# Performance work log

Measured on AMD Instinct MI355X. Metric: run time of the kernel, lower is better.

Reference implementation:

```python
import jax, jax.numpy as jnp
import numpy as np

N = 100000      # nodes
NNZ = 1600000   # edges (avg degree 16)
F_IN = 128
F_OUT = 128


def setup_inputs() -> dict:
    key = jax.random.key(0)
    ks = jax.random.split(key, 8)
    return {
        "features": jax.random.normal(ks[0], (N, F_IN), dtype=jnp.float32),
        "edge_val": jax.random.uniform(ks[1], (NNZ,), dtype=jnp.float32),
        "W1": jax.random.normal(ks[2], (F_IN, F_OUT), dtype=jnp.float32) * 0.05,
        "b1": jax.random.normal(ks[3], (F_OUT,), dtype=jnp.float32) * 0.05,
        "W2": jax.random.normal(ks[4], (F_IN, F_OUT), dtype=jnp.float32) * 0.05,
        "b2": jax.random.normal(ks[5], (F_OUT,), dtype=jnp.float32) * 0.05,
        "edge_row": jax.random.randint(ks[6], (NNZ,), 0, N, dtype=jnp.int32),
        "edge_col": jax.random.randint(ks[7], (NNZ,), 0, N, dtype=jnp.int32),
    }


def _spmm(edge_val, edge_row, edge_col, x, n):
    # sparse (n,n) COO matrix @ dense (n,f): gather cols, scale, scatter-add rows
    gathered = edge_val[:, None] * x[edge_col]          # (nnz, f)
    return jax.ops.segment_sum(gathered, edge_row, num_segments=n)


def reference(features, edge_val, W1, b1, W2, b2, edge_row, edge_col):
    n = features.shape[0]
    Lf = _spmm(edge_val, edge_row, edge_col, features, n)   # L2 @ features
    inter_feature = Lf * features                            # elementwise mul
    # L1 = L + I, so L1 @ features == Lf + features (selfLoop is identity)
    inter_part1 = (Lf + features) @ W1 + b1                  # self.linear
    Li = _spmm(edge_val, edge_row, edge_col, inter_feature, n)
    inter_part2 = Li @ W2 + b2                               # interActTransform
    return inter_part1 + inter_part2
```

## Files before the change

kernel.cpp:

```cpp
#include <hip/hip_runtime.h>

#define F 128
#define NBSHIFT 7
#define CAPB 3072
#define CHUNK 8192

typedef __attribute__((ext_vector_type(8))) short bf16x8;
typedef __attribute__((ext_vector_type(4))) float f32x4;

__device__ inline float bf2f(unsigned short u) {
    union { unsigned int i; float f; } x;
    x.i = ((unsigned int)u) << 16;
    return x.f;
}
__device__ inline unsigned short f2bf(float f) {
    union { float f; unsigned int i; } x;
    x.f = f;
    unsigned int lsb = (x.i >> 16) & 1;
    x.i += 0x7FFFu + lsb;
    return (unsigned short)(x.i >> 16);
}

__global__ __launch_bounds__(256) void convert_feat(
    const float* __restrict__ feat, unsigned short* __restrict__ feat_h, int total4)
{
    int i = blockIdx.x * 256 + threadIdx.x;
    if (i >= total4) return;
    float4 v = *(const float4*)(feat + (size_t)i * 4);
    ushort4 o;
    o.x = f2bf(v.x); o.y = f2bf(v.y); o.z = f2bf(v.z); o.w = f2bf(v.w);
    *(ushort4*)(feat_h + (size_t)i * 4) = o;
}

__global__ __launch_bounds__(256) void pack_W(
    const float* __restrict__ W1, const float* __restrict__ W2,
    unsigned short* __restrict__ Wp)
{
    int idx = blockIdx.x * 256 + threadIdx.x;
    if (idx >= 8 * 8 * 64) return;
    int lane = idx & 63;
    int ks   = (idx >> 6) & 7;
    int nt   = idx >> 9;
    int col  = nt * 16 + (lane & 15);
    int krow = ks * 32 + (lane >> 4) * 8;
    const float* W = (krow < 128) ? (W1 + (size_t)krow * F)
                                  : (W2 + (size_t)(krow - 128) * F);
    unsigned short o[8];
#pragma unroll
    for (int j = 0; j < 8; ++j) o[j] = f2bf(W[(size_t)j * F + col]);
    unsigned short* dst = Wp + (size_t)idx * 8;
    *(ushort4*)(dst)     = make_ushort4(o[0], o[1], o[2], o[3]);
    *(ushort4*)(dst + 4) = make_ushort4(o[4], o[5], o[6], o[7]);
}

__global__ __launch_bounds__(256) void bin_edges(
    const int* __restrict__ er, const int* __restrict__ ec,
    const float* __restrict__ ev,
    int* __restrict__ gcnt, uint2* __restrict__ gbuf, int nnz, int nb)
{
    __shared__ int hist[1024];
    __shared__ int base[1024];
    const int tid  = threadIdx.x;
    const int e0   = blockIdx.x * CHUNK;
    const int eend = min(e0 + CHUNK, nnz);

    for (int b = tid; b < nb; b += 256) hist[b] = 0;
    __syncthreads();

    for (int e = e0 + tid; e < eend; e += 256) {
        int b = er[e] >> NBSHIFT;
        atomicAdd(&hist[b], 1);
    }
    __syncthreads();

    for (int b = tid; b < nb; b += 256) {
        int h = hist[b];
        base[b] = h ? atomicAdd(&gcnt[b], h) : 0;
        hist[b] = 0;
    }
    __syncthreads();

    for (int e = e0 + tid; e < eend; e += 256) {
        int r = er[e];
        int b = r >> NBSHIFT;
        int rank = atomicAdd(&hist[b], 1);
        int idx  = base[b] + rank;
        if (idx >= CAPB) idx = CAPB - 1;
        unsigned int q = (unsigned int)__float2int_rn(ev[e] * 32767.f);
        gbuf[(size_t)b * CAPB + idx] =
            make_uint2((q << 17) | (unsigned int)ec[e], (unsigned int)r);
    }
}

__global__ __launch_bounds__(256) void bucket_to_rows(
    const int* __restrict__ gcnt, const uint2* __restrict__ gbuf,
    int* __restrict__ cnt, unsigned int* __restrict__ recs, int n, int cap)
{
    __shared__ unsigned int slots[128][64];
    __shared__ int lcnt[128];
    const int b = blockIdx.x;
    const int tid = threadIdx.x;
    const int base_row = b << NBSHIFT;

    for (int r = tid; r < 128; r += 256) lcnt[r] = 0;
    __syncthreads();

    int nrec = gcnt[b];
    if (nrec > CAPB) nrec = CAPB;
    const uint2* gb = gbuf + (size_t)b * CAPB;
    for (int i = tid; i < nrec; i += 256) {
        uint2 rec = gb[i];
        int r = (int)rec.y - base_row;
        int pos = atomicAdd(&lcnt[r], 1);
        if (pos < cap) slots[r][pos] = rec.x;
    }
    __syncthreads();

    int r = tid >> 1;
    int row = base_row + r;
    if (row < n) {
        int c = lcnt[r];
        if (c > cap) c = cap;
        if ((tid & 1) == 0) cnt[row] = c;
        unsigned int* dst = recs + (size_t)row * cap;
        for (int i = tid & 1; i < c; i += 2) dst[i] = slots[r][i];
    }
}

__global__ __launch_bounds__(256) void spmm_feat(
    const unsigned short* __restrict__ feat_h, const float* __restrict__ feat,
    const int* __restrict__ cnt, const unsigned int* __restrict__ recs,
    unsigned short* __restrict__ A1_h, unsigned short* __restrict__ P_h,
    int n, int cap)
{
    int gid = blockIdx.x * 256 + threadIdx.x;
    int row = gid >> 5;
    if (row >= n) return;
    int f = (gid & 31) << 2;
    const unsigned int* rp = recs + (size_t)row * cap;
    int e = cnt[row];
    if (e > cap) e = cap;

    float4 acc0 = {0.f, 0.f, 0.f, 0.f};
    float4 acc1 = {0.f, 0.f, 0.f, 0.f};
    int i = 0;
    for (; i + 1 < e; i += 2) {
        unsigned int u0 = rp[i];
        unsigned int u1 = rp[i + 1];
        float v0 = (float)(u0 >> 17) * (1.f / 32767.f);
        float v1 = (float)(u1 >> 17) * (1.f / 32767.f);
        ushort4 x0 = *(const ushort4*)(feat_h + (size_t)(u0 & 0x1FFFF) * F + f);
        ushort4 x1 = *(const ushort4*)(feat_h + (size_t)(u1 & 0x1FFFF) * F + f);
        acc0.x += v0 * bf2f(x0.x);
        acc0.y += v0 * bf2f(x0.y);
        acc0.z += v0 * bf2f(x0.z);
        acc0.w += v0 * bf2f(x0.w);
        acc1.x += v1 * bf2f(x1.x);
        acc1.y += v1 * bf2f(x1.y);
        acc1.z += v1 * bf2f(x1.z);
        acc1.w += v1 * bf2f(x1.w);
    }
    if (i < e) {
        unsigned int u0 = rp[i];
        float v0 = (float)(u0 >> 17) * (1.f / 32767.f);
        ushort4 x0 = *(const ushort4*)(feat_h + (size_t)(u0 & 0x1FFFF) * F + f);
        acc0.x += v0 * bf2f(x0.x);
        acc0.y += v0 * bf2f(x0.y);
        acc0.z += v0 * bf2f(x0.z);
        acc0.w += v0 * bf2f(x0.w);
    }
    float4 acc;
    acc.x = acc0.x + acc1.x;
    acc.y = acc0.y + acc1.y;
    acc.z = acc0.z + acc1.z;
    acc.w = acc0.w + acc1.w;

    size_t o = (size_t)row * F + f;
    float4 ft = *(const float4*)(feat + o);

    ushort4 a1;
    a1.x = f2bf(acc.x + ft.x);
    a1.y = f2bf(acc.y + ft.y);
    a1.z = f2bf(acc.z + ft.z);
    a1.w = f2bf(acc.w + ft.w);
    *(ushort4*)(A1_h + o) = a1;

    ushort4 ph;
    ph.x = f2bf(acc.x * ft.x);
    ph.y = f2bf(acc.y * ft.y);
    ph.z = f2bf(acc.z * ft.z);
    ph.w = f2bf(acc.w * ft.w);
    *(ushort4*)(P_h + o) = ph;
}

__global__ __launch_bounds__(256) void spmm_inter(
    const unsigned short* __restrict__ P_h,
    const int* __restrict__ cnt, const unsigned int* __restrict__ recs,
    unsigned short* __restrict__ Li_h, int n, int cap)
{
    int gid = blockIdx.x * 256 + threadIdx.x;
    int row = gid >> 5;
    if (row >= n) return;
    int f = (gid & 31) << 2;
    const unsigned int* rp = recs + (size_t)row * cap;
    int e = cnt[row];
    if (e > cap) e = cap;

    float4 acc0 = {0.f, 0.f, 0.f, 0.f};
    float4 acc1 = {0.f, 0.f, 0.f, 0.f};
    int i = 0;
    for (; i + 1 < e; i += 2) {
        unsigned int u0 = rp[i];
        unsigned int u1 = rp[i + 1];
        float v0 = (float)(u0 >> 17) * (1.f / 32767.f);
        float v1 = (float)(u1 >> 17) * (1.f / 32767.f);
        ushort4 x0 = *(const ushort4*)(P_h + (size_t)(u0 & 0x1FFFF) * F + f);
        ushort4 x1 = *(const ushort4*)(P_h + (size_t)(u1 & 0x1FFFF) * F + f);
        acc0.x += v0 * bf2f(x0.x);
        acc0.y += v0 * bf2f(x0.y);
        acc0.z += v0 * bf2f(x0.z);
        acc0.w += v0 * bf2f(x0.w);
        acc1.x += v1 * bf2f(x1.x);
        acc1.y += v1 * bf2f(x1.y);
        acc1.z += v1 * bf2f(x1.z);
        acc1.w += v1 * bf2f(x1.w);
    }
    if (i < e) {
        unsigned int u0 = rp[i];
        float v0 = (float)(u0 >> 17) * (1.f / 32767.f);
        ushort4 x0 = *(const ushort4*)(P_h + (size_t)(u0 & 0x1FFFF) * F + f);
        acc0.x += v0 * bf2f(x0.x);
        acc0.y += v0 * bf2f(x0.y);
        acc0.z += v0 * bf2f(x0.z);
        acc0.w += v0 * bf2f(x0.w);
    }
    ushort4 lh;
    lh.x = f2bf(acc0.x + acc1.x);
    lh.y = f2bf(acc0.y + acc1.y);
    lh.z = f2bf(acc0.z + acc1.z);
    lh.w = f2bf(acc0.w + acc1.w);
    *(ushort4*)(Li_h + (size_t)row * F + f) = lh;
}

__global__ __launch_bounds__(256) void gemm_mfma(
    const unsigned short* __restrict__ A1_h,
    const unsigned short* __restrict__ Li_h,
    const unsigned short* __restrict__ Wp,
    const float* __restrict__ b1, const float* __restrict__ b2,
    float* __restrict__ out, int n)
{
    const int wave = threadIdx.x >> 6;
    const int lane = threadIdx.x & 63;
    const int quad = lane >> 4;
    const int l16  = lane & 15;
    const int row0 = blockIdx.x * 64 + wave * 16;

    int arow = row0 + l16;
    if (arow >= n) arow = n - 1;

    f32x4 acc[8];
#pragma unroll
    for (int t = 0; t < 8; ++t) acc[t] = (f32x4){0.f, 0.f, 0.f, 0.f};

    const unsigned short* A1p = A1_h + (size_t)arow * F + quad * 8;
    const unsigned short* A2p = Li_h + (size_t)arow * F + quad * 8;

#pragma unroll
    for (int ks = 0; ks < 8; ++ks) {
        const unsigned short* ap = (ks < 4) ? (A1p + ks * 32) : (A2p + (ks - 4) * 32);
        bf16x8 a = *(const bf16x8*)ap;
#pragma unroll
        for (int t = 0; t < 8; ++t) {
            bf16x8 b = *(const bf16x8*)(Wp + ((size_t)(t * 8 + ks) * 64 + lane) * 8);
            acc[t] = __builtin_amdgcn_mfma_f32_16x16x32_bf16(a, b, acc[t], 0, 0, 0);
        }
    }

    const int orow0 = row0 + quad * 4;
#pragma unroll
    for (int t = 0; t < 8; ++t) {
        int col = t * 16 + l16;
        float bias = b1[col] + b2[col];
#pragma unroll
        for (int r = 0; r < 4; ++r) {
            int gr = orow0 + r;
            if (gr < n) out[(size_t)gr * F + col] = acc[t][r] + bias;
        }
    }
}

extern "C" void kernel_launch(void* const* d_in, const int* in_sizes, int n_in,
                              void* d_out, int out_size, void* d_ws, size_t ws_size,
                              hipStream_t stream)
{
    const float* feat = (const float*)d_in[0];
    const float* ev   = (const float*)d_in[1];
    const float* W1   = (const float*)d_in[2];
    const float* b1   = (const float*)d_in[3];
    const float* W2   = (const float*)d_in[4];
    const float* b2   = (const float*)d_in[5];
    const int*   er   = (const int*)d_in[6];
    const int*   ec   = (const int*)d_in[7];

    const int n   = in_sizes[0] / F;
    const int nnz = in_sizes[1];
    int nb = (n + 127) >> NBSHIFT;
    if (nb > 1024) nb = 1024;

    char* ws = (char*)d_ws;
    unsigned short* feat_h = (unsigned short*)ws;  ws += (size_t)n * F * sizeof(short);
    unsigned short* A1_h   = (unsigned short*)ws;  ws += (size_t)n * F * sizeof(short);
    unsigned short* P_h    = (unsigned short*)ws;  ws += (size_t)n * F * sizeof(short);
    unsigned short* Li_h   = (unsigned short*)ws;  ws += (size_t)n * F * sizeof(short);
    unsigned short* Wp     = (unsigned short*)ws;  ws += (size_t)8 * 8 * 64 * 8 * sizeof(short);
    int* cnt               = (int*)ws;             ws += (size_t)n * sizeof(int);
    int* gcnt              = (int*)ws;             ws += (size_t)nb * sizeof(int);
    unsigned int* recs     = (unsigned int*)ws;

    uint2* gbuf = (uint2*)Li_h;

    size_t used  = (size_t)(ws - (char*)d_ws);
    size_t avail = (ws_size > used) ? (ws_size - used) : 0;
    int cap = (int)(avail / ((size_t)n * sizeof(unsigned int)));
    if (cap > 64) cap = 64;

    hipMemsetAsync(gcnt, 0, (size_t)nb * sizeof(int), stream);

    const int total4 = n * F / 4;

    convert_feat<<<(total4 + 255) / 256, 256, 0, stream>>>(feat, feat_h, total4);
    pack_W<<<16, 256, 0, stream>>>(W1, W2, Wp);

    bin_edges<<<(nnz + CHUNK - 1) / CHUNK, 256, 0, stream>>>(er, ec, ev, gcnt,
                                                             gbuf, nnz, nb);
    bucket_to_rows<<<nb, 256, 0, stream>>>(gcnt, gbuf, cnt, recs, n, cap);

    int spmm_blocks = (n * 32 + 255) / 256;
    spmm_feat<<<spmm_blocks, 256, 0, stream>>>(feat_h, feat, cnt, recs,
                                               A1_h, P_h, n, cap);
    spmm_inter<<<spmm_blocks, 256, 0, stream>>>(P_h, cnt, recs, Li_h, n, cap);

    gemm_mfma<<<(n + 63) / 64, 256, 0, stream>>>(A1_h, Li_h, Wp, b1, b2,
                                                 (float*)d_out, n);
}
```

Baseline: 388.3 us.

## Fuse prep kernels, vectorize row record stores, and unroll SpMM gathers by eight

Feature conversion, weight packing and edge binning now run as one launch, with block index ranges choosing the job. Binning keeps row ids in registers instead of reading them twice. Row records are written with 128-bit stores from a padded shared tile, with cap rounded down to a multiple of four. The SpMM gather loop loads records as uint4 and issues eight independent feature gathers into four accumulators, to get more memory requests in flight. The costs are more register pressure and a less balanced fused launch.

```diff
diff --git a/kernel.cpp b/kernel.cpp
--- a/kernel.cpp
+++ b/kernel.cpp
@@ -4,6 +4,7 @@
 #define NBSHIFT 7
 #define CAPB 3072
 #define CHUNK 8192
+#define NBMAX 1024
 
 typedef __attribute__((ext_vector_type(8))) short bf16x8;
 typedef __attribute__((ext_vector_type(4))) float f32x4;
@@ -21,74 +22,81 @@
     return (unsigned short)(x.i >> 16);
 }
 
-__global__ __launch_bounds__(256) void convert_feat(
-    const float* __restrict__ feat, unsigned short* __restrict__ feat_h, int total4)
-{
-    int i = blockIdx.x * 256 + threadIdx.x;
-    if (i >= total4) return;
-    float4 v = *(const float4*)(feat + (size_t)i * 4);
-    ushort4 o;
-    o.x = f2bf(v.x); o.y = f2bf(v.y); o.z = f2bf(v.z); o.w = f2bf(v.w);
-    *(ushort4*)(feat_h + (size_t)i * 4) = o;
-}
-
-__global__ __launch_bounds__(256) void pack_W(
+__global__ __launch_bounds__(256) void prep(
+    const float* __restrict__ feat, unsigned short* __restrict__ feat_h, int total4,
     const float* __restrict__ W1, const float* __restrict__ W2,
-    unsigned short* __restrict__ Wp)
-{
-    int idx = blockIdx.x * 256 + threadIdx.x;
-    if (idx >= 8 * 8 * 64) return;
-    int lane = idx & 63;
-    int ks   = (idx >> 6) & 7;
-    int nt   = idx >> 9;
-    int col  = nt * 16 + (lane & 15);
-    int krow = ks * 32 + (lane >> 4) * 8;
-    const float* W = (krow < 128) ? (W1 + (size_t)krow * F)
-                                  : (W2 + (size_t)(krow - 128) * F);
-    unsigned short o[8];
-#pragma unroll
-    for (int j = 0; j < 8; ++j) o[j] = f2bf(W[(size_t)j * F + col]);
-    unsigned short* dst = Wp + (size_t)idx * 8;
-    *(ushort4*)(dst)     = make_ushort4(o[0], o[1], o[2], o[3]);
-    *(ushort4*)(dst + 4) = make_ushort4(o[4], o[5], o[6], o[7]);
-}
-
-__global__ __launch_bounds__(256) void bin_edges(
+    unsigned short* __restrict__ Wp,
     const int* __restrict__ er, const int* __restrict__ ec,
     const float* __restrict__ ev,
-    int* __restrict__ gcnt, uint2* __restrict__ gbuf, int nnz, int nb)
-{
-    __shared__ int hist[1024];
-    __shared__ int base[1024];
-    const int tid  = threadIdx.x;
-    const int e0   = blockIdx.x * CHUNK;
-    const int eend = min(e0 + CHUNK, nnz);
-
-    for (int b = tid; b < nb; b += 256) hist[b] = 0;
-    __syncthreads();
-
-    for (int e = e0 + tid; e < eend; e += 256) {
-        int b = er[e] >> NBSHIFT;
-        atomicAdd(&hist[b], 1);
-    }
-    __syncthreads();
-
-    for (int b = tid; b < nb; b += 256) {
-        int h = hist[b];
-        base[b] = h ? atomicAdd(&gcnt[b], h) : 0;
-        hist[b] = 0;
-    }
-    __syncthreads();
-
-    for (int e = e0 + tid; e < eend; e += 256) {
-        int r = er[e];
-        int b = r >> NBSHIFT;
-        int rank = atomicAdd(&hist[b], 1);
-        int idx  = base[b] + rank;
-        if (idx >= CAPB) idx = CAPB - 1;
-        unsigned int q = (unsigned int)__float2int_rn(ev[e] * 32767.f);
-        gbuf[(size_t)b * CAPB + idx] =
-            make_uint2((q << 17) | (unsigned int)ec[e], (unsigned int)r);
+    int* __restrict__ gcnt, uint2* __restrict__ gbuf, int nnz, int nb, int nbin)
+{
+    __shared__ int hist[NBMAX];
+    __shared__ int base[NBMAX];
+    const int bid = blockIdx.x;
+    const int tid = threadIdx.x;
+
+    if (bid < nbin) {
+        const int e0 = bid * CHUNK;
+        int rreg[32];
+
+        for (int b = tid; b < nb; b += 256) hist[b] = 0;
+        __syncthreads();
+
+#pragma unroll
+        for (int k = 0; k < 32; ++k) {
+            int e = e0 + k * 256 + tid;
+            int r = (e < nnz) ? er[e] : -1;
+            rreg[k] = r;
+            if (r >= 0) atomicAdd(&hist[r >> NBSHIFT], 1);
+        }
+        __syncthreads();
+
+        for (int b = tid; b < nb; b += 256) {
+            int h = hist[b];
+            base[b] = h ? atomicAdd(&gcnt[b], h) : 0;
+            hist[b] = 0;
+        }
+        __syncthreads();
+
+#pragma unroll
+        for (int k = 0; k < 32; ++k) {
+            int r = rreg[k];
+            if (r >= 0) {
+                int e = e0 + k * 256 + tid;
+                int b = r >> NBSHIFT;
+                int rank = atomicAdd(&hist[b], 1);
+                int idx  = base[b] + rank;
+                if (idx >= CAPB) idx = CAPB - 1;
+                unsigned int q = (unsigned int)__float2int_rn(ev[e] * 32767.f);
+                gbuf[(size_t)b * CAPB + idx] =
+                    make_uint2((q << 17) | (unsigned int)ec[e], (unsigned int)r);
+            }
+        }
+    } else if (bid < nbin + 16) {
+        int idx = (bid - nbin) * 256 + tid;
+        if (idx < 8 * 8 * 64) {
+            int lane = idx & 63;
+            int ks   = (idx >> 6) & 7;
+            int nt   = idx >> 9;
+            int col  = nt * 16 + (lane & 15);
+            int krow = ks * 32 + (lane >> 4) * 8;
+            const float* W = (krow < 128) ? (W1 + (size_t)krow * F)
+                                          : (W2 + (size_t)(krow - 128) * F);
+            unsigned short o[8];
+#pragma unroll
+            for (int j = 0; j < 8; ++j) o[j] = f2bf(W[(size_t)j * F + col]);
+            unsigned short* dst = Wp + (size_t)idx * 8;
+            *(ushort4*)(dst)     = make_ushort4(o[0], o[1], o[2], o[3]);
+            *(ushort4*)(dst + 4) = make_ushort4(o[4], o[5], o[6], o[7]);
+        }
+    } else {
+        int i = (bid - nbin - 16) * 256 + tid;
+        if (i < total4) {
+            float4 v = *(const float4*)(feat + (size_t)i * 4);
+            ushort4 o;
+            o.x = f2bf(v.x); o.y = f2bf(v.y); o.z = f2bf(v.z); o.w = f2bf(v.w);
+            *(ushort4*)(feat_h + (size_t)i * 4) = o;
+        }
     }
 }
 
@@ -96,7 +104,7 @@
     const int* __restrict__ gcnt, const uint2* __restrict__ gbuf,
     int* __restrict__ cnt, unsigned int* __restrict__ recs, int n, int cap)
 {
-    __shared__ unsigned int slots[128][64];
+    __shared__ unsigned int slots[128][68];
     __shared__ int lcnt[128];
     const int b = blockIdx.x;
     const int tid = threadIdx.x;
@@ -116,15 +124,94 @@
     }
     __syncthreads();
 
-    int r = tid >> 1;
-    int row = base_row + r;
-    if (row < n) {
-        int c = lcnt[r];
+    const int sub = tid & 3;
+    for (int rr = tid >> 2; rr < 128; rr += 64) {
+        int row = base_row + rr;
+        if (row >= n) continue;
+        int c = lcnt[rr];
         if (c > cap) c = cap;
-        if ((tid & 1) == 0) cnt[row] = c;
-        unsigned int* dst = recs + (size_t)row * cap;
-        for (int i = tid & 1; i < c; i += 2) dst[i] = slots[r][i];
-    }
+        if (sub == 0) cnt[row] = c;
+        uint4* dst = (uint4*)(recs + (size_t)row * cap);
+        for (int q = sub; q * 4 < c; q += 4)
+            dst[q] = *(const uint4*)&slots[rr][q * 4];
+    }
+}
+
+__device__ inline float4 row_gather(
+    const unsigned short* __restrict__ src,
+    const unsigned int* __restrict__ rp, int e, int f)
+{
+    float4 A0 = {0.f,0.f,0.f,0.f}, A1 = {0.f,0.f,0.f,0.f};
+    float4 A2 = {0.f,0.f,0.f,0.f}, A3 = {0.f,0.f,0.f,0.f};
+    int i = 0;
+    for (; i + 7 < e; i += 8) {
+        uint4 ua = *(const uint4*)(rp + i);
+        uint4 ub = *(const uint4*)(rp + i + 4);
+        ushort4 x0 = *(const ushort4*)(src + (size_t)(ua.x & 0x1FFFF) * F + f);
+        ushort4 x1 = *(const ushort4*)(src + (size_t)(ua.y & 0x1FFFF) * F + f);
+        ushort4 x2 = *(const ushort4*)(src + (size_t)(ua.z & 0x1FFFF) * F + f);
+        ushort4 x3 = *(const ushort4*)(src + (size_t)(ua.w & 0x1FFFF) * F + f);
+        ushort4 x4 = *(const ushort4*)(src + (size_t)(ub.x & 0x1FFFF) * F + f);
+        ushort4 x5 = *(const ushort4*)(src + (size_t)(ub.y & 0x1FFFF) * F + f);
+        ushort4 x6 = *(const ushort4*)(src + (size_t)(ub.z & 0x1FFFF) * F + f);
+        ushort4 x7 = *(const ushort4*)(src + (size_t)(ub.w & 0x1FFFF) * F + f);
+        float v0 = (float)(ua.x >> 17) * (1.f / 32767.f);
+        float v1 = (float)(ua.y >> 17) * (1.f / 32767.f);
+        float v2 = (float)(ua.z >> 17) * (1.f / 32767.f);
+        float v3 = (float)(ua.w >> 17) * (1.f / 32767.f);
+        float v4 = (float)(ub.x >> 17) * (1.f / 32767.f);
+        float v5 = (float)(ub.y >> 17) * (1.f / 32767.f);
+        float v6 = (float)(ub.z >> 17) * (1.f / 32767.f);
+        float v7 = (float)(ub.w >> 17) * (1.f / 32767.f);
+        A0.x += v0 * bf2f(x0.x); A0.y += v0 * bf2f(x0.y);
+        A0.z += v0 * bf2f(x0.z); A0.w += v0 * bf2f(x0.w);
+        A1.x += v1 * bf2f(x1.x); A1.y += v1 * bf2f(x1.y);
+        A1.z += v1 * bf2f(x1.z); A1.w += v1 * bf2f(x1.w);
+        A2.x += v2 * bf2f(x2.x); A2.y += v2 * bf2f(x2.y);
+        A2.z += v2 * bf2f(x2.z); A2.w += v2 * bf2f(x2.w);
+        A3.x += v3 * bf2f(x3.x); A3.y += v3 * bf2f(x3.y);
+        A3.z += v3 * bf2f(x3.z); A3.w += v3 * bf2f(x3.w);
+        A0.x += v4 * bf2f(x4.x); A0.y += v4 * bf2f(x4.y);
+        A0.z += v4 * bf2f(x4.z); A0.w += v4 * bf2f(x4.w);
+        A1.x += v5 * bf2f(x5.x); A1.y += v5 * bf2f(x5.y);
+        A1.z += v5 * bf2f(x5.z); A1.w += v5 * bf2f(x5.w);
+        A2.x += v6 * bf2f(x6.x); A2.y += v6 * bf2f(x6.y);
+        A2.z += v6 * bf2f(x6.z); A2.w += v6 * bf2f(x6.w);
+        A3.x += v7 * bf2f(x7.x); A3.y += v7 * bf2f(x7.y);
+        A3.z += v7 * bf2f(x7.z); A3.w += v7 * bf2f(x7.w);
+    }
+    for (; i + 3 < e; i += 4) {
+        uint4 ua = *(const uint4*)(rp + i);
+        ushort4 x0 = *(const ushort4*)(src + (size_t)(ua.x & 0x1FFFF) * F + f);
+        ushort4 x1 = *(const ushort4*)(src + (size_t)(ua.y & 0x1FFFF) * F + f);
+        ushort4 x2 = *(const ushort4*)(src + (size_t)(ua.z & 0x1FFFF) * F + f);
+        ushort4 x3 = *(const ushort4*)(src + (size_t)(ua.w & 0x1FFFF) * F + f);
+        float v0 = (float)(ua.x >> 17) * (1.f / 32767.f);
+        float v1 = (float)(ua.y >> 17) * (1.f / 32767.f);
+        float v2 = (float)(ua.z >> 17) * (1.f / 32767.f);
+        float v3 = (float)(ua.w >> 17) * (1.f / 32767.f);
+        A0.x += v0 * bf2f(x0.x); A0.y += v0 * bf2f(x0.y);
+        A0.z += v0 * bf2f(x0.z); A0.w += v0 * bf2f(x0.w);
+        A1.x += v1 * bf2f(x1.x); A1.y += v1 * bf2f(x1.y);
+        A1.z += v1 * bf2f(x1.z); A1.w += v1 * bf2f(x1.w);
+        A2.x += v2 * bf2f(x2.x); A2.y += v2 * bf2f(x2.y);
+        A2.z += v2 * bf2f(x2.z); A2.w += v2 * bf2f(x2.w);
+        A3.x += v3 * bf2f(x3.x); A3.y += v3 * bf2f(x3.y);
+        A3.z += v3 * bf2f(x3.z); A3.w += v3 * bf2f(x3.w);
+    }
+    for (; i < e; ++i) {
+        unsigned int u0 = rp[i];
+        float v0 = (float)(u0 >> 17) * (1.f / 32767.f);
+        ushort4 x0 = *(const ushort4*)(src + (size_t)(u0 & 0x1FFFF) * F + f);
+        A0.x += v0 * bf2f(x0.x); A0.y += v0 * bf2f(x0.y);
+        A0.z += v0 * bf2f(x0.z); A0.w += v0 * bf2f(x0.w);
+    }
+    float4 acc;
+    acc.x = (A0.x + A1.x) + (A2.x + A3.x);
+    acc.y = (A0.y + A1.y) + (A2.y + A3.y);
+    acc.z = (A0.z + A1.z) + (A2.z + A3.z);
+    acc.w = (A0.w + A1.w) + (A2.w + A3.w);
+    return acc;
 }
 
 __global__ __launch_bounds__(256) void spmm_feat(
@@ -137,43 +224,9 @@
     int row = gid >> 5;
     if (row >= n) return;
     int f = (gid & 31) << 2;
-    const unsigned int* rp = recs + (size_t)row * cap;
     int e = cnt[row];
     if (e > cap) e = cap;
-
-    float4 acc0 = {0.f, 0.f, 0.f, 0.f};
-    float4 acc1 = {0.f, 0.f, 0.f, 0.f};
-    int i = 0;
-    for (; i + 1 < e; i += 2) {
-        unsigned int u0 = rp[i];
-        unsigned int u1 = rp[i + 1];
-        float v0 = (float)(u0 >> 17) * (1.f / 32767.f);
-        float v1 = (float)(u1 >> 17) * (1.f / 32767.f);
-        ushort4 x0 = *(const ushort4*)(feat_h + (size_t)(u0 & 0x1FFFF) * F + f);
-        ushort4 x1 = *(const ushort4*)(feat_h + (size_t)(u1 & 0x1FFFF) * F + f);
-        acc0.x += v0 * bf2f(x0.x);
-        acc0.y += v0 * bf2f(x0.y);
-        acc0.z += v0 * bf2f(x0.z);
-        acc0.w += v0 * bf2f(x0.w);
-        acc1.x += v1 * bf2f(x1.x);
-        acc1.y += v1 * bf2f(x1.y);
-        acc1.z += v1 * bf2f(x1.z);
-        acc1.w += v1 * bf2f(x1.w);
-    }
-    if (i < e) {
-        unsigned int u0 = rp[i];
-        float v0 = (float)(u0 >> 17) * (1.f / 32767.f);
-        ushort4 x0 = *(const ushort4*)(feat_h + (size_t)(u0 & 0x1FFFF) * F + f);
-        acc0.x += v0 * bf2f(x0.x);
-        acc0.y += v0 * bf2f(x0.y);
-        acc0.z += v0 * bf2f(x0.z);
-        acc0.w += v0 * bf2f(x0.w);
-    }
-    float4 acc;
-    acc.x = acc0.x + acc1.x;
-    acc.y = acc0.y + acc1.y;
-    acc.z = acc0.z + acc1.z;
-    acc.w = acc0.w + acc1.w;
+    float4 acc = row_gather(feat_h, recs + (size_t)row * cap, e, f);
 
     size_t o = (size_t)row * F + f;
     float4 ft = *(const float4*)(feat + o);
@@ -202,43 +255,15 @@
     int row = gid >> 5;
     if (row >= n) return;
     int f = (gid & 31) << 2;
-    const unsigned int* rp = recs + (size_t)row * cap;
     int e = cnt[row];
     if (e > cap) e = cap;
-
-    float4 acc0 = {0.f, 0.f, 0.f, 0.f};
-    float4 acc1 = {0.f, 0.f, 0.f, 0.f};
-    int i = 0;
-    for (; i + 1 < e; i += 2) {
-        unsigned int u0 = rp[i];
-        unsigned int u1 = rp[i + 1];
-        float v0 = (float)(u0 >> 17) * (1.f / 32767.f);
-        float v1 = (float)(u1 >> 17) * (1.f / 32767.f);
-        ushort4 x0 = *(const ushort4*)(P_h + (size_t)(u0 & 0x1FFFF) * F + f);
-        ushort4 x1 = *(const ushort4*)(P_h + (size_t)(u1 & 0x1FFFF) * F + f);
-        acc0.x += v0 * bf2f(x0.x);
-        acc0.y += v0 * bf2f(x0.y);
-        acc0.z += v0 * bf2f(x0.z);
-        acc0.w += v0 * bf2f(x0.w);
-        acc1.x += v1 * bf2f(x1.x);
-        acc1.y += v1 * bf2f(x1.y);
-        acc1.z += v1 * bf2f(x1.z);
-        acc1.w += v1 * bf2f(x1.w);
-    }
-    if (i < e) {
-        unsigned int u0 = rp[i];
-        float v0 = (float)(u0 >> 17) * (1.f / 32767.f);
-        ushort4 x0 = *(const ushort4*)(P_h + (size_t)(u0 & 0x1FFFF) * F + f);
-        acc0.x += v0 * bf2f(x0.x);
-        acc0.y += v0 * bf2f(x0.y);
-        acc0.z += v0 * bf2f(x0.z);
-        acc0.w += v0 * bf2f(x0.w);
-    }
+    float4 acc = row_gather(P_h, recs + (size_t)row * cap, e, f);
+
     ushort4 lh;
-    lh.x = f2bf(acc0.x + acc1.x);
-    lh.y = f2bf(acc0.y + acc1.y);
-    lh.z = f2bf(acc0.z + acc1.z);
-    lh.w = f2bf(acc0.w + acc1.w);
+    lh.x = f2bf(acc.x);
+    lh.y = f2bf(acc.y);
+    lh.z = f2bf(acc.z);
+    lh.w = f2bf(acc.w);
     *(ushort4*)(Li_h + (size_t)row * F + f) = lh;
 }
 
@@ -305,7 +330,7 @@
     const int n   = in_sizes[0] / F;
     const int nnz = in_sizes[1];
     int nb = (n + 127) >> NBSHIFT;
-    if (nb > 1024) nb = 1024;
+    if (nb > NBMAX) nb = NBMAX;
 
     char* ws = (char*)d_ws;
     unsigned short* feat_h = (unsigned short*)ws;  ws += (size_t)n * F * sizeof(short);
@@ -323,16 +348,16 @@
     size_t avail = (ws_size > used) ? (ws_size - used) : 0;
     int cap = (int)(avail / ((size_t)n * sizeof(unsigned int)));
     if (cap > 64) cap = 64;
+    cap &= ~3;
 
     hipMemsetAsync(gcnt, 0, (size_t)nb * sizeof(int), stream);
 
     const int total4 = n * F / 4;
-
-    convert_feat<<<(total4 + 255) / 256, 256, 0, stream>>>(feat, feat_h, total4);
-    pack_W<<<16, 256, 0, stream>>>(W1, W2, Wp);
-
-    bin_edges<<<(nnz + CHUNK - 1) / CHUNK, 256, 0, stream>>>(er, ec, ev, gcnt,
-                                                             gbuf, nnz, nb);
+    const int nbin = (nnz + CHUNK - 1) / CHUNK;
+    const int conv_blocks = (total4 + 255) / 256;
+    prep<<<nbin + 16 + conv_blocks, 256, 0, stream>>>(
+        feat, feat_h, total4, W1, W2, Wp, er, ec, ev, gcnt, gbuf, nnz, nb, nbin);
+
     bucket_to_rows<<<nb, 256, 0, stream>>>(gcnt, gbuf, cnt, recs, n, cap);
 
     int spmm_blocks = (n * 32 + 255) / 256;
```

Result: faster. 346.5 us (-10.8%).
